# Performance work log

Measured on AMD Instinct MI355X. Metric: run time of the kernel, lower is better.

Reference implementation:

```python
import jax, jax.numpy as jnp
import numpy as np

B, S, H, I, E, K = 4, 1024, 1024, 768, 8, 2


def setup_inputs() -> dict:
    key = jax.random.key(0)
    ks = jax.random.split(key, 6)
    return {
        "hidden_states": jax.random.normal(ks[0], (B, S, H), dtype=jnp.float32),
        "routing_weights": jax.random.uniform(ks[1], (B, S, K), dtype=jnp.float32),
        "selected_experts": jax.random.randint(ks[2], (B, S, K), 0, E, dtype=jnp.int64),
        "gate_weight": jax.random.normal(ks[3], (E, I, H), dtype=jnp.float32) * 0.02,
        "up_weight": jax.random.normal(ks[4], (E, I, H), dtype=jnp.float32) * 0.02,
        "down_weight": jax.random.normal(ks[5], (E, H, I), dtype=jnp.float32) * 0.02,
    }


def reference(hidden_states, routing_weights, selected_experts, gate_weight, up_weight, down_weight):
    b, s, h = hidden_states.shape
    x = hidden_states.reshape(-1, h)                    # [T, H]
    T = x.shape[0]
    k = selected_experts.shape[-1]
    rw = routing_weights.astype(x.dtype).reshape(T, k)  # [T, K]
    se = selected_experts.reshape(T, k)                 # [T, K]
    e_total = gate_weight.shape[0]
    # combine[t, e] = sum of routing weights of slots of token t routed to expert e
    # (equivalent to the original per-slot dispatch + weighted scatter-add combine)
    combine = jnp.zeros((T, e_total), dtype=x.dtype).at[jnp.arange(T)[:, None], se].add(rw)
    out = jnp.zeros_like(x)
    for e in range(e_total):  # small fixed expert count
        g = x @ gate_weight[e].T                        # [T, I]
        u = x @ up_weight[e].T                          # [T, I]
        y = (jax.nn.silu(g) * u) @ down_weight[e].T     # [T, H]
        out = out + combine[:, e:e + 1] * y
    return out.reshape(b, s, h)
```

## Files before the change

kernel.cpp:

```cpp
#include <hip/hip_runtime.h>
#include <hip/hip_bf16.h>

typedef __attribute__((ext_vector_type(8))) short bf16x8;
typedef __attribute__((ext_vector_type(8))) ushort ushort8;
typedef __attribute__((ext_vector_type(4))) float f32x4;

#define T_TOK 4096
#define HDIM  1024
#define IDIM  768
#define NEXP  8
#define TOPK  2
#define NSLOT (T_TOK * TOPK)

#define BM  128
#define BN  128
#define BKS 32

#define NX4 (T_TOK * HDIM / 4)
#define NW4 (NEXP * IDIM * HDIM / 4)
#define NX8 (NX4 / 2)
#define NW8 (NW4 / 2)

__device__ __forceinline__ ushort f2bf(float f) {
  union { __hip_bfloat16 h; ushort u; } cv;
  cv.h = __float2bfloat16(f);
  return cv.u;
}
__device__ __forceinline__ float bf2f(ushort u) {
  union { float f; uint v; } cv; cv.v = ((uint)u) << 16; return cv.f;
}

__device__ __forceinline__ void gload_lds16(const ushort* g, ushort* l) {
  __builtin_amdgcn_global_load_lds(
      (const __attribute__((address_space(1))) void*)g,
      (__attribute__((address_space(3))) void*)l, 16, 0, 0);
}

__global__ void cvt_route(const float* __restrict__ hs, const float* __restrict__ gw,
                          const float* __restrict__ uw, const float* __restrict__ dw,
                          ushort* __restrict__ xb, ushort* __restrict__ gwb,
                          ushort* __restrict__ uwb, ushort* __restrict__ dwb,
                          const int* __restrict__ sel, int* __restrict__ counts,
                          int* __restrict__ toklist) {
  int bid = blockIdx.x;
  if (bid < 32) {
    int slot = bid * 256 + threadIdx.x;
    int e = sel[slot];
    int idx = atomicAdd(&counts[e], 1);
    toklist[e * NSLOT + idx] = slot;
    return;
  }
  int i = (bid - 32) * 256 + threadIdx.x;
  const float* src; ushort* dst; int off;
  if (i < NX8) { src = hs; dst = xb; off = i; }
  else {
    int j = i - NX8;
    if (j < NW8)            { src = gw; dst = gwb; off = j; }
    else if (j < 2 * NW8)   { src = uw; dst = uwb; off = j - NW8; }
    else                    { src = dw; dst = dwb; off = j - 2 * NW8; }
  }
  const float4* s4 = reinterpret_cast<const float4*>(src) + 2 * (size_t)off;
  float4 v0 = s4[0];
  float4 v1 = s4[1];
  ushort8 o;
  o[0] = f2bf(v0.x); o[1] = f2bf(v0.y); o[2] = f2bf(v0.z); o[3] = f2bf(v0.w);
  o[4] = f2bf(v1.x); o[5] = f2bf(v1.y); o[6] = f2bf(v1.z); o[7] = f2bf(v1.w);
  reinterpret_cast<ushort8*>(dst)[off] = o;
}


__launch_bounds__(256, 2)
__global__ void gemm_gateup(const ushort* __restrict__ xb,
                            const ushort* __restrict__ gwb,
                            const ushort* __restrict__ uwb,
                            const int* __restrict__ counts,
                            const int* __restrict__ toklist,
                            ushort* __restrict__ act) {
  const int b = blockIdx.x;
  const int e = b & 7;
  const int r = b >> 3;
  const int nt = r % 6, mt = r / 6;
  const int cnt = counts[e];
  const int m0 = mt * BM;
  if (m0 >= cnt) return;
  const int n0 = nt * BN;

  __shared__ __align__(16) ushort As[2][BM * BKS];
  __shared__ __align__(16) ushort Bgs[2][BM * BKS];
  __shared__ __align__(16) ushort Bus[2][BM * BKS];

  const int tid = threadIdx.x;
  const int wave = tid >> 6, lane = tid & 63;
  const int wm = wave >> 1, wn = wave & 1;
  const int lrow = lane & 15, lk16 = lane >> 4;
  const int rl = lane >> 2;
  const int gck = ((lane & 3) ^ ((lane >> 3) & 3)) << 3;

  const int ent0 = m0 + wave * 16 + rl;
  const int ent1 = ent0 + 64;
  const int arow0 = (ent0 < cnt) ? (toklist[e * NSLOT + ent0] >> 1) : 0;
  const int arow1 = (ent1 < cnt) ? (toklist[e * NSLOT + ent1] >> 1) : 0;
  const int brow0 = wave * 16 + rl;
  const int brow1 = brow0 + 64;

  const ushort* aP0 = xb + (size_t)arow0 * HDIM + gck;
  const ushort* aP1 = xb + (size_t)arow1 * HDIM + gck;
  const ushort* wBase = gwb + (size_t)e * IDIM * HDIM;
  const ushort* gP0 = wBase + (size_t)(n0 + brow0) * HDIM + gck;
  const ushort* gP1 = wBase + (size_t)(n0 + brow1) * HDIM + gck;
  const ushort* uBase = uwb + (size_t)e * IDIM * HDIM;
  const ushort* uP0 = uBase + (size_t)(n0 + brow0) * HDIM + gck;
  const ushort* uP1 = uBase + (size_t)(n0 + brow1) * HDIM + gck;

  f32x4 accg[4][4], accu[4][4];
  const f32x4 fzero = {0.f, 0.f, 0.f, 0.f};
  #pragma unroll
  for (int a = 0; a < 4; ++a)
    #pragma unroll
    for (int c = 0; c < 4; ++c) { accg[a][c] = fzero; accu[a][c] = fzero; }

  auto stage = [&](int buf, int k0) {
    gload_lds16(aP0 + k0, &As[buf][wave * 512]);
    gload_lds16(aP1 + k0, &As[buf][(wave + 4) * 512]);
    gload_lds16(gP0 + k0, &Bgs[buf][wave * 512]);
    gload_lds16(gP1 + k0, &Bgs[buf][(wave + 4) * 512]);
    gload_lds16(uP0 + k0, &Bus[buf][wave * 512]);
    gload_lds16(uP1 + k0, &Bus[buf][(wave + 4) * 512]);
  };

  const int swzc = ((lk16 ^ ((lrow >> 1) & 3)) << 3);
  auto compute = [&](int buf) {
    bf16x8 aF[4], bgF[4], buF[4];
    #pragma unroll
    for (int mi = 0; mi < 4; ++mi) {
      int rr = wm * 64 + mi * 16 + lrow;
      aF[mi] = *reinterpret_cast<const bf16x8*>(&As[buf][rr * 32 + swzc]);
    }
    #pragma unroll
    for (int ni = 0; ni < 4; ++ni) {
      int rr = wn * 64 + ni * 16 + lrow;
      bgF[ni] = *reinterpret_cast<const bf16x8*>(&Bgs[buf][rr * 32 + swzc]);
      buF[ni] = *reinterpret_cast<const bf16x8*>(&Bus[buf][rr * 32 + swzc]);
    }
    #pragma unroll
    for (int mi = 0; mi < 4; ++mi)
      #pragma unroll
      for (int ni = 0; ni < 4; ++ni) {
        accg[mi][ni] = __builtin_amdgcn_mfma_f32_16x16x32_bf16(aF[mi], bgF[ni], accg[mi][ni], 0, 0, 0);
        accu[mi][ni] = __builtin_amdgcn_mfma_f32_16x16x32_bf16(aF[mi], buF[ni], accu[mi][ni], 0, 0, 0);
      }
  };

  stage(0, 0);
  __syncthreads();
  #pragma unroll 1
  for (int t = 0; t < HDIM / BKS; t += 2) {
    if (t + 1 < HDIM / BKS) stage(1, (t + 1) * BKS);
    compute(0);
    __syncthreads();
    if (t + 2 < HDIM / BKS) stage(0, (t + 2) * BKS);
    compute(1);
    __syncthreads();
  }

  const int lcol = lane & 15;
  const int lrb = (lane >> 4) * 4;
  #pragma unroll
  for (int mi = 0; mi < 4; ++mi)
    #pragma unroll
    for (int j = 0; j < 4; ++j) {
      int row = wm * 64 + mi * 16 + lrb + j;
      int entry = m0 + row;
      if (entry >= cnt) continue;
      int slot = toklist[e * NSLOT + entry];
      #pragma unroll
      for (int ni = 0; ni < 4; ++ni) {
        int col = n0 + wn * 64 + ni * 16 + lcol;
        float g = accg[mi][ni][j];
        float u = accu[mi][ni][j];
        float y = (g / (1.0f + __expf(-g))) * u;
        act[(size_t)slot * IDIM + col] = f2bf(y);
      }
    }
}

__launch_bounds__(256, 3)
__global__ void gemm_down(const ushort* __restrict__ act,
                          const ushort* __restrict__ dwb,
                          const int* __restrict__ counts,
                          const int* __restrict__ toklist,
                          ushort* __restrict__ yact) {
  const int b = blockIdx.x;
  const int e = b & 7;
  const int r = b >> 3;
  const int nt = r & 7, mt = r >> 3;
  const int cnt = counts[e];
  const int m0 = mt * BM;
  if (m0 >= cnt) return;
  const int n0 = nt * BN;

  __shared__ __align__(16) ushort As[2][BM * BKS];
  __shared__ __align__(16) ushort Bs[2][BM * BKS];

  const int tid = threadIdx.x;
  const int wave = tid >> 6, lane = tid & 63;
  const int wm = wave >> 1, wn = wave & 1;
  const int lrow = lane & 15, lk16 = lane >> 4;
  const int rl = lane >> 2;
  const int gck = ((lane & 3) ^ ((lane >> 3) & 3)) << 3;

  const int ent0 = m0 + wave * 16 + rl;
  const int ent1 = ent0 + 64;
  const int arow0 = (ent0 < cnt) ? toklist[e * NSLOT + ent0] : 0;
  const int arow1 = (ent1 < cnt) ? toklist[e * NSLOT + ent1] : 0;
  const int brow0 = wave * 16 + rl;
  const int brow1 = brow0 + 64;

  const ushort* aP0 = act + (size_t)arow0 * IDIM + gck;
  const ushort* aP1 = act + (size_t)arow1 * IDIM + gck;
  const ushort* dBase = dwb + (size_t)e * HDIM * IDIM;
  const ushort* dP0 = dBase + (size_t)(n0 + brow0) * IDIM + gck;
  const ushort* dP1 = dBase + (size_t)(n0 + brow1) * IDIM + gck;

  f32x4 acc[4][4];
  const f32x4 fzero = {0.f, 0.f, 0.f, 0.f};
  #pragma unroll
  for (int a = 0; a < 4; ++a)
    #pragma unroll
    for (int c = 0; c < 4; ++c) acc[a][c] = fzero;

  auto stage = [&](int buf, int k0) {
    gload_lds16(aP0 + k0, &As[buf][wave * 512]);
    gload_lds16(aP1 + k0, &As[buf][(wave + 4) * 512]);
    gload_lds16(dP0 + k0, &Bs[buf][wave * 512]);
    gload_lds16(dP1 + k0, &Bs[buf][(wave + 4) * 512]);
  };

  const int swzc = ((lk16 ^ ((lrow >> 1) & 3)) << 3);
  auto compute = [&](int buf) {
    bf16x8 aF[4], bF[4];
    #pragma unroll
    for (int mi = 0; mi < 4; ++mi) {
      int rr = wm * 64 + mi * 16 + lrow;
      aF[mi] = *reinterpret_cast<const bf16x8*>(&As[buf][rr * 32 + swzc]);
    }
    #pragma unroll
    for (int ni = 0; ni < 4; ++ni) {
      int rr = wn * 64 + ni * 16 + lrow;
      bF[ni] = *reinterpret_cast<const bf16x8*>(&Bs[buf][rr * 32 + swzc]);
    }
    #pragma unroll
    for (int mi = 0; mi < 4; ++mi)
      #pragma unroll
      for (int ni = 0; ni < 4; ++ni)
        acc[mi][ni] = __builtin_amdgcn_mfma_f32_16x16x32_bf16(aF[mi], bF[ni], acc[mi][ni], 0, 0, 0);
  };

  stage(0, 0);
  __syncthreads();
  #pragma unroll 1
  for (int t = 0; t < IDIM / BKS; t += 2) {
    if (t + 1 < IDIM / BKS) stage(1, (t + 1) * BKS);
    compute(0);
    __syncthreads();
    if (t + 2 < IDIM / BKS) stage(0, (t + 2) * BKS);
    compute(1);
    __syncthreads();
  }

  const int lcol = lane & 15;
  const int lrb = (lane >> 4) * 4;
  #pragma unroll
  for (int mi = 0; mi < 4; ++mi)
    #pragma unroll
    for (int j = 0; j < 4; ++j) {
      int row = wm * 64 + mi * 16 + lrb + j;
      int entry = m0 + row;
      if (entry >= cnt) continue;
      int slot = toklist[e * NSLOT + entry];
      #pragma unroll
      for (int ni = 0; ni < 4; ++ni) {
        int col = n0 + wn * 64 + ni * 16 + lcol;
        yact[(size_t)slot * HDIM + col] = f2bf(acc[mi][ni][j]);
      }
    }
}

__global__ void combine_kernel(const ushort* __restrict__ yact, const float* __restrict__ rw,
                               float* __restrict__ out) {
  int i = blockIdx.x * blockDim.x + threadIdx.x;
  int t = i >> 7;
  int h0 = (i & 127) << 3;
  const bf16x8 y0 = *reinterpret_cast<const bf16x8*>(yact + (size_t)(2 * t) * HDIM + h0);
  const bf16x8 y1 = *reinterpret_cast<const bf16x8*>(yact + (size_t)(2 * t + 1) * HDIM + h0);
  float w0 = rw[2 * t], w1 = rw[2 * t + 1];
  float o[8];
  #pragma unroll
  for (int j = 0; j < 8; ++j)
    o[j] = w0 * bf2f((ushort)y0[j]) + w1 * bf2f((ushort)y1[j]);
  float4* op = reinterpret_cast<float4*>(out + (size_t)t * HDIM + h0);
  op[0] = make_float4(o[0], o[1], o[2], o[3]);
  op[1] = make_float4(o[4], o[5], o[6], o[7]);
}

extern "C" void kernel_launch(void* const* d_in, const int* in_sizes, int n_in,
                              void* d_out, int out_size, void* d_ws, size_t ws_size,
                              hipStream_t stream) {
  const float* hs = (const float*)d_in[0];
  const float* rw = (const float*)d_in[1];
  const int*   se = (const int*)d_in[2];
  const float* gw = (const float*)d_in[3];
  const float* uw = (const float*)d_in[4];
  const float* dw = (const float*)d_in[5];
  float* out = (float*)d_out;

  char* base = (char*)d_ws;
  ushort* xb      = (ushort*)(base + 0);
  ushort* gwb     = (ushort*)(base + 8388608);
  ushort* uwb     = (ushort*)(base + 20971520);
  ushort* dwb     = (ushort*)(base + 33554432);
  ushort* act     = (ushort*)(base + 46137344);
  ushort* yact    = (ushort*)(base + 8388608);
  int*    toklist = (int*)(base + 58720256);
  int*    counts  = (int*)(base + 58982400);

  hipMemsetAsync(counts, 0, 256, stream);

  int total8 = NX8 + 3 * NW8;
  cvt_route<<<32 + (total8 + 255) / 256, 256, 0, stream>>>(hs, gw, uw, dw, xb, gwb, uwb, dwb,
                                                           se, counts, toklist);
  gemm_gateup<<<8 * 6 * (NSLOT / BM), 256, 0, stream>>>(xb, gwb, uwb, counts, toklist, act);
  gemm_down<<<8 * 8 * (NSLOT / BM), 256, 0, stream>>>(act, dwb, counts, toklist, yact);
  combine_kernel<<<T_TOK * HDIM / 8 / 256, 256, 0, stream>>>(yact, rw, out);
}
```

Baseline: 224.8 us.

## Fuse fp32-to-bf16 weight conversion into GEMM tile loading

Removes the separate pass that converted the gate, up and down weights to bf16. The GEMM kernels now load fp32 weight tiles into registers, convert them to bf16, and store them into LDS. Loads are issued before the MFMA compute and committed to LDS after it, to hide latency. This avoids a full read/write pass over all expert weights, but doubles the weight bytes each tile fetches, drops the async global_load_lds path for weights, and adds register pressure in the gate/up kernel.

After: 238.7 us. +6.2%, slower.

```diff
diff --git a/kernel.cpp b/kernel.cpp
--- a/kernel.cpp
+++ b/kernel.cpp
@@ -16,10 +16,7 @@
 #define BN  128
 #define BKS 32
 
-#define NX4 (T_TOK * HDIM / 4)
-#define NW4 (NEXP * IDIM * HDIM / 4)
-#define NX8 (NX4 / 2)
-#define NW8 (NW4 / 2)
+#define NX8 (T_TOK * HDIM / 8)
 
 __device__ __forceinline__ ushort f2bf(float f) {
   union { __hip_bfloat16 h; ushort u; } cv;
@@ -36,12 +33,16 @@
       (__attribute__((address_space(3))) void*)l, 16, 0, 0);
 }
 
-__global__ void cvt_route(const float* __restrict__ hs, const float* __restrict__ gw,
-                          const float* __restrict__ uw, const float* __restrict__ dw,
-                          ushort* __restrict__ xb, ushort* __restrict__ gwb,
-                          ushort* __restrict__ uwb, ushort* __restrict__ dwb,
-                          const int* __restrict__ sel, int* __restrict__ counts,
-                          int* __restrict__ toklist) {
+__device__ __forceinline__ ushort8 pack_bf16(float4 a, float4 b) {
+  ushort8 o;
+  o[0] = f2bf(a.x); o[1] = f2bf(a.y); o[2] = f2bf(a.z); o[3] = f2bf(a.w);
+  o[4] = f2bf(b.x); o[5] = f2bf(b.y); o[6] = f2bf(b.z); o[7] = f2bf(b.w);
+  return o;
+}
+
+__global__ void cvt_x_route(const float* __restrict__ hs, ushort* __restrict__ xb,
+                            const int* __restrict__ sel, int* __restrict__ counts,
+                            int* __restrict__ toklist) {
   int bid = blockIdx.x;
   if (bid < 32) {
     int slot = bid * 256 + threadIdx.x;
@@ -51,28 +52,17 @@
     return;
   }
   int i = (bid - 32) * 256 + threadIdx.x;
-  const float* src; ushort* dst; int off;
-  if (i < NX8) { src = hs; dst = xb; off = i; }
-  else {
-    int j = i - NX8;
-    if (j < NW8)            { src = gw; dst = gwb; off = j; }
-    else if (j < 2 * NW8)   { src = uw; dst = uwb; off = j - NW8; }
-    else                    { src = dw; dst = dwb; off = j - 2 * NW8; }
-  }
-  const float4* s4 = reinterpret_cast<const float4*>(src) + 2 * (size_t)off;
+  const float4* s4 = reinterpret_cast<const float4*>(hs) + 2 * (size_t)i;
   float4 v0 = s4[0];
   float4 v1 = s4[1];
-  ushort8 o;
-  o[0] = f2bf(v0.x); o[1] = f2bf(v0.y); o[2] = f2bf(v0.z); o[3] = f2bf(v0.w);
-  o[4] = f2bf(v1.x); o[5] = f2bf(v1.y); o[6] = f2bf(v1.z); o[7] = f2bf(v1.w);
-  reinterpret_cast<ushort8*>(dst)[off] = o;
+  reinterpret_cast<ushort8*>(xb)[i] = pack_bf16(v0, v1);
 }
 
 
 __launch_bounds__(256, 2)
 __global__ void gemm_gateup(const ushort* __restrict__ xb,
-                            const ushort* __restrict__ gwb,
-                            const ushort* __restrict__ uwb,
+                            const float* __restrict__ gw,
+                            const float* __restrict__ uw,
                             const int* __restrict__ counts,
                             const int* __restrict__ toklist,
                             ushort* __restrict__ act) {
@@ -105,12 +95,10 @@
 
   const ushort* aP0 = xb + (size_t)arow0 * HDIM + gck;
   const ushort* aP1 = xb + (size_t)arow1 * HDIM + gck;
-  const ushort* wBase = gwb + (size_t)e * IDIM * HDIM;
-  const ushort* gP0 = wBase + (size_t)(n0 + brow0) * HDIM + gck;
-  const ushort* gP1 = wBase + (size_t)(n0 + brow1) * HDIM + gck;
-  const ushort* uBase = uwb + (size_t)e * IDIM * HDIM;
-  const ushort* uP0 = uBase + (size_t)(n0 + brow0) * HDIM + gck;
-  const ushort* uP1 = uBase + (size_t)(n0 + brow1) * HDIM + gck;
+  const float* gP0 = gw + (size_t)e * IDIM * HDIM + (size_t)(n0 + brow0) * HDIM + gck;
+  const float* gP1 = gw + (size_t)e * IDIM * HDIM + (size_t)(n0 + brow1) * HDIM + gck;
+  const float* uP0 = uw + (size_t)e * IDIM * HDIM + (size_t)(n0 + brow0) * HDIM + gck;
+  const float* uP1 = uw + (size_t)e * IDIM * HDIM + (size_t)(n0 + brow1) * HDIM + gck;
 
   f32x4 accg[4][4], accu[4][4];
   const f32x4 fzero = {0.f, 0.f, 0.f, 0.f};
@@ -119,13 +107,25 @@
     #pragma unroll
     for (int c = 0; c < 4; ++c) { accg[a][c] = fzero; accu[a][c] = fzero; }
 
-  auto stage = [&](int buf, int k0) {
+  float4 vgl0, vgl1, vgh0, vgh1, vul0, vul1, vuh0, vuh1;
+
+  auto issue = [&](int buf, int k0) {
     gload_lds16(aP0 + k0, &As[buf][wave * 512]);
     gload_lds16(aP1 + k0, &As[buf][(wave + 4) * 512]);
-    gload_lds16(gP0 + k0, &Bgs[buf][wave * 512]);
-    gload_lds16(gP1 + k0, &Bgs[buf][(wave + 4) * 512]);
-    gload_lds16(uP0 + k0, &Bus[buf][wave * 512]);
-    gload_lds16(uP1 + k0, &Bus[buf][(wave + 4) * 512]);
+    const float4* g0 = reinterpret_cast<const float4*>(gP0 + k0);
+    const float4* g1 = reinterpret_cast<const float4*>(gP1 + k0);
+    const float4* u0 = reinterpret_cast<const float4*>(uP0 + k0);
+    const float4* u1 = reinterpret_cast<const float4*>(uP1 + k0);
+    vgl0 = g0[0]; vgl1 = g0[1];
+    vgh0 = g1[0]; vgh1 = g1[1];
+    vul0 = u0[0]; vul1 = u0[1];
+    vuh0 = u1[0]; vuh1 = u1[1];
+  };
+  auto commit = [&](int buf) {
+    *reinterpret_cast<ushort8*>(&Bgs[buf][wave * 512 + lane * 8]) = pack_bf16(vgl0, vgl1);
+    *reinterpret_cast<ushort8*>(&Bgs[buf][(wave + 4) * 512 + lane * 8]) = pack_bf16(vgh0, vgh1);
+    *reinterpret_cast<ushort8*>(&Bus[buf][wave * 512 + lane * 8]) = pack_bf16(vul0, vul1);
+    *reinterpret_cast<ushort8*>(&Bus[buf][(wave + 4) * 512 + lane * 8]) = pack_bf16(vuh0, vuh1);
   };
 
   const int swzc = ((lk16 ^ ((lrow >> 1) & 3)) << 3);
@@ -151,15 +151,19 @@
       }
   };
 
-  stage(0, 0);
+  const int NT = HDIM / BKS;
+  issue(0, 0);
+  commit(0);
   __syncthreads();
   #pragma unroll 1
-  for (int t = 0; t < HDIM / BKS; t += 2) {
-    if (t + 1 < HDIM / BKS) stage(1, (t + 1) * BKS);
+  for (int t = 0; t < NT; t += 2) {
+    if (t + 1 < NT) issue(1, (t + 1) * BKS);
     compute(0);
+    if (t + 1 < NT) commit(1);
     __syncthreads();
-    if (t + 2 < HDIM / BKS) stage(0, (t + 2) * BKS);
+    if (t + 2 < NT) issue(0, (t + 2) * BKS);
     compute(1);
+    if (t + 2 < NT) commit(0);
     __syncthreads();
   }
 
@@ -186,7 +190,7 @@
 
 __launch_bounds__(256, 3)
 __global__ void gemm_down(const ushort* __restrict__ act,
-                          const ushort* __restrict__ dwb,
+                          const float* __restrict__ dw,
                           const int* __restrict__ counts,
                           const int* __restrict__ toklist,
                           ushort* __restrict__ yact) {
@@ -218,9 +222,8 @@
 
   const ushort* aP0 = act + (size_t)arow0 * IDIM + gck;
   const ushort* aP1 = act + (size_t)arow1 * IDIM + gck;
-  const ushort* dBase = dwb + (size_t)e * HDIM * IDIM;
-  const ushort* dP0 = dBase + (size_t)(n0 + brow0) * IDIM + gck;
-  const ushort* dP1 = dBase + (size_t)(n0 + brow1) * IDIM + gck;
+  const float* dP0 = dw + (size_t)e * HDIM * IDIM + (size_t)(n0 + brow0) * IDIM + gck;
+  const float* dP1 = dw + (size_t)e * HDIM * IDIM + (size_t)(n0 + brow1) * IDIM + gck;
 
   f32x4 acc[4][4];
   const f32x4 fzero = {0.f, 0.f, 0.f, 0.f};
@@ -229,11 +232,19 @@
     #pragma unroll
     for (int c = 0; c < 4; ++c) acc[a][c] = fzero;
 
-  auto stage = [&](int buf, int k0) {
+  float4 vdl0, vdl1, vdh0, vdh1;
+
+  auto issue = [&](int buf, int k0) {
     gload_lds16(aP0 + k0, &As[buf][wave * 512]);
     gload_lds16(aP1 + k0, &As[buf][(wave + 4) * 512]);
-    gload_lds16(dP0 + k0, &Bs[buf][wave * 512]);
-    gload_lds16(dP1 + k0, &Bs[buf][(wave + 4) * 512]);
+    const float4* d0 = reinterpret_cast<const float4*>(dP0 + k0);
+    const float4* d1 = reinterpret_cast<const float4*>(dP1 + k0);
+    vdl0 = d0[0]; vdl1 = d0[1];
+    vdh0 = d1[0]; vdh1 = d1[1];
+  };
+  auto commit = [&](int buf) {
+    *reinterpret_cast<ushort8*>(&Bs[buf][wave * 512 + lane * 8]) = pack_bf16(vdl0, vdl1);
+    *reinterpret_cast<ushort8*>(&Bs[buf][(wave + 4) * 512 + lane * 8]) = pack_bf16(vdh0, vdh1);
   };
 
   const int swzc = ((lk16 ^ ((lrow >> 1) & 3)) << 3);
@@ -256,15 +267,19 @@
         acc[mi][ni] = __builtin_amdgcn_mfma_f32_16x16x32_bf16(aF[mi], bF[ni], acc[mi][ni], 0, 0, 0);
   };
 
-  stage(0, 0);
+  const int NT = IDIM / BKS;
+  issue(0, 0);
+  commit(0);
   __syncthreads();
   #pragma unroll 1
-  for (int t = 0; t < IDIM / BKS; t += 2) {
-    if (t + 1 < IDIM / BKS) stage(1, (t + 1) * BKS);
+  for (int t = 0; t < NT; t += 2) {
+    if (t + 1 < NT) issue(1, (t + 1) * BKS);
     compute(0);
+    if (t + 1 < NT) commit(1);
     __syncthreads();
-    if (t + 2 < IDIM / BKS) stage(0, (t + 2) * BKS);
+    if (t + 2 < NT) issue(0, (t + 2) * BKS);
     compute(1);
+    if (t + 2 < NT) commit(0);
     __syncthreads();
   }
 
@@ -316,20 +331,15 @@
 
   char* base = (char*)d_ws;
   ushort* xb      = (ushort*)(base + 0);
-  ushort* gwb     = (ushort*)(base + 8388608);
-  ushort* uwb     = (ushort*)(base + 20971520);
-  ushort* dwb     = (ushort*)(base + 33554432);
-  ushort* act     = (ushort*)(base + 46137344);
-  ushort* yact    = (ushort*)(base + 8388608);
-  int*    toklist = (int*)(base + 58720256);
-  int*    counts  = (int*)(base + 58982400);
+  ushort* act     = (ushort*)(base + 8388608);
+  ushort* yact    = (ushort*)(base + 20971520);
+  int*    toklist = (int*)(base + 37748736);
+  int*    counts  = (int*)(base + 38010880);
 
   hipMemsetAsync(counts, 0, 256, stream);
 
-  int total8 = NX8 + 3 * NW8;
-  cvt_route<<<32 + (total8 + 255) / 256, 256, 0, stream>>>(hs, gw, uw, dw, xb, gwb, uwb, dwb,
-                                                           se, counts, toklist);
-  gemm_gateup<<<8 * 6 * (NSLOT / BM), 256, 0, stream>>>(xb, gwb, uwb, counts, toklist, act);
-  gemm_down<<<8 * 8 * (NSLOT / BM), 256, 0, stream>>>(act, dwb, counts, toklist, yact);
+  cvt_x_route<<<32 + NX8 / 256, 256, 0, stream>>>(hs, xb, se, counts, toklist);
+  gemm_gateup<<<8 * 6 * (NSLOT / BM), 256, 0, stream>>>(xb, gw, uw, counts, toklist, act);
+  gemm_down<<<8 * 8 * (NSLOT / BM), 256, 0, stream>>>(act, dw, counts, toklist, yact);
   combine_kernel<<<T_TOK * HDIM / 8 / 256, 256, 0, stream>>>(yact, rw, out);
 }
```
